# Performance work log

Hardware: AMD Instinct MI355X
Metric: run time of the kernel (lower is better)

Reference implementation:

```python
import jax, jax.numpy as jnp
import numpy as np

B, IN, OUT, NUM_F = 131072, 128, 128, 8


def setup_inputs() -> dict:
    key = jax.random.key(0)
    ks = jax.random.split(key, 6)
    x = jax.random.normal(ks[0], (B, IN), dtype=jnp.float32)
    grid = jnp.arange(NUM_F, dtype=jnp.float32) + 1.0            # nn.Parameter(arange(num_f)+1)
    base_weight = jax.random.normal(ks[1], (OUT, IN), dtype=jnp.float32) * 0.05
    scale_sp = jnp.ones((OUT,), dtype=jnp.float32)
    coef = jax.random.uniform(ks[2], (IN, NUM_F), dtype=jnp.float32)  # torch.rand
    # Conv1d(in=IN*NUM_F, out=OUT*NUM_F, k=1, groups=NUM_F) == per-frequency [OUT, IN] matmul
    fan_in = IN  # per-group in-channels * kernel_size(1)
    bound = 1.0 / np.sqrt(fan_in)
    conv_w = jax.random.uniform(ks[3], (NUM_F, OUT, IN), dtype=jnp.float32,
                                minval=-bound, maxval=bound)
    conv_b = jax.random.uniform(ks[4], (NUM_F, OUT), dtype=jnp.float32,
                                minval=-bound, maxval=bound)
    return {"x": x, "grid": grid, "base_weight": base_weight,
            "scale_sp": scale_sp, "coef": coef, "conv_w": conv_w, "conv_b": conv_b}


def reference(x, grid, base_weight, scale_sp, coef, conv_w, conv_b):
    # base path: SiLU(x) @ W_base^T  -> [B, OUT]
    base_out = jax.nn.silu(x) @ base_weight.T
    # Fourier basis: sin(grid_f * x_i) -> [B, F, I]
    s = jnp.sin(x[:, None, :] * grid[None, :, None])
    # coef [I, F] broadcast-multiplied per (i, f)
    s = s * coef.T[None, :, :]                      # [B, F, I]
    # grouped 1x1 conv == per-frequency matmul, plus per-(f, o) bias
    spline = jnp.einsum('bfi,foi->bfo', s, conv_w) + conv_b[None, :, :]  # [B, F, OUT]
    spline_out = spline.sum(axis=1) * scale_sp      # [B, OUT]
    return base_out + spline_out
```

## Files before the change

kernel.cpp:

```cpp
#include <hip/hip_runtime.h>
#include <stdint.h>

#define NCHUNK 9
#define IN_DIM 128
#define OUT_DIM 128
#define NUM_F 8
#define B_TOTAL 131072

#define WBASE_ELEMS (OUT_DIM * IN_DIM)
#define WSIN_ELEMS (8 * OUT_DIM * IN_DIM)
#define SLICE 16384

typedef _Float16 hf16x8 __attribute__((ext_vector_type(8)));
typedef float floatx16 __attribute__((ext_vector_type(16)));

typedef __attribute__((address_space(1))) const unsigned int gas_u32;
typedef __attribute__((address_space(3))) unsigned int las_u32;

__device__ __forceinline__ unsigned short f2h_rn(float f) {
  _Float16 h = (_Float16)f;
  return __builtin_bit_cast(unsigned short, h);
}

__global__ void skan_prep(const float* __restrict__ base_w,
                          const float* __restrict__ scale_sp,
                          const float* __restrict__ coef,
                          const float* __restrict__ conv_w,
                          const float* __restrict__ conv_b,
                          unsigned short* __restrict__ Wbase,
                          unsigned short* __restrict__ Wsin,
                          float* __restrict__ bias) {
  int b = blockIdx.x;
  int i = threadIdx.x;
  int j = i & 7, q2 = (i >> 3) & 1;
  if (b < NCHUNK * OUT_DIM) {
    int c = b >> 7;
    int o = b & 127;
    if (c == 0) {
      float v = base_w[o * IN_DIM + i];
      Wbase[((i >> 4) * 2 + q2) * 1024 + o * 8 + j] = f2h_rn(v);
    } else {
      int f = c - 1;
      float v = conv_w[(f * OUT_DIM + o) * IN_DIM + i] * coef[i * NUM_F + f] * scale_sp[o];
      Wsin[((i >> 4) * 16 + f * 2 + q2) * 1024 + o * 8 + j] = f2h_rn(v);
    }
  } else {
    float s = 0.f;
#pragma unroll
    for (int f = 0; f < NUM_F; ++f) s += conv_b[f * OUT_DIM + i];
    bias[i] = s * scale_sp[i];
  }
}

__device__ __forceinline__ hf16x8 hpack(const float* v) {
  union { unsigned u[4]; hf16x8 f; } r;
  r.u[0] = __builtin_bit_cast(unsigned, __builtin_amdgcn_cvt_pkrtz(v[0], v[1]));
  r.u[1] = __builtin_bit_cast(unsigned, __builtin_amdgcn_cvt_pkrtz(v[2], v[3]));
  r.u[2] = __builtin_bit_cast(unsigned, __builtin_amdgcn_cvt_pkrtz(v[4], v[5]));
  r.u[3] = __builtin_bit_cast(unsigned, __builtin_amdgcn_cvt_pkrtz(v[6], v[7]));
  return r.f;
}

__device__ __forceinline__ float silu(float v) {
  return v * __builtin_amdgcn_rcpf(1.f + __expf(-v));
}

__global__ __launch_bounds__(256, 3)
void skan_main(const float* __restrict__ x,
               const unsigned short* __restrict__ Wbase,
               const unsigned short* __restrict__ Wsin,
               const float* __restrict__ bias,
               float* __restrict__ out) {
  __shared__ unsigned short sB[SLICE];

  const int tid  = threadIdx.x;
  const int lane = tid & 63;
  const int w    = tid >> 6;
  const int m    = lane & 31;
  const int q2   = lane >> 5;
  const int waveRow = blockIdx.x * 128 + w * 32;

  const int colOff = m * 8;

  floatx16 acc[4];
#pragma unroll
  for (int nt = 0; nt < 4; ++nt)
#pragma unroll
    for (int e = 0; e < 16; ++e) acc[nt][e] = 0.f;

  const float* xr = x + (size_t)(waveRow + m) * IN_DIM;

#pragma unroll 1
  for (int p = 0; p < 8; ++p) {
    {
      const char* src = (const char*)(Wsin + p * SLICE);
      char* dst = (char*)sB;
      int off = tid * 16;
#pragma unroll
      for (int it = 0; it < 8; ++it) {
        __builtin_amdgcn_global_load_lds((gas_u32*)(src + off), (las_u32*)(dst + off),
                                         16, 0, 0);
        off += 4096;
      }
    }

    float xv[8];
    {
      float4 a = *(const float4*)(xr + p * 16 + q2 * 8);
      float4 b = *(const float4*)(xr + p * 16 + q2 * 8 + 4);
      xv[0] = a.x; xv[1] = a.y; xv[2] = a.z; xv[3] = a.w;
      xv[4] = b.x; xv[5] = b.y; xv[6] = b.z; xv[7] = b.w;
    }

    {
      int4 Bb[4];
#pragma unroll
      for (int nt = 0; nt < 4; ++nt)
        Bb[nt] = *(const int4*)(Wbase + (p * 2 + q2) * 1024 + colOff + nt * 256);
      float sv[8];
#pragma unroll
      for (int j = 0; j < 8; ++j) sv[j] = silu(xv[j]);
      hf16x8 a0 = hpack(sv);
#pragma unroll
      for (int nt = 0; nt < 4; ++nt) {
        hf16x8 bf = __builtin_bit_cast(hf16x8, Bb[nt]);
        acc[nt] = __builtin_amdgcn_mfma_f32_32x32x16_f16(a0, bf, acc[nt], 0, 0, 0);
      }
    }

    __syncthreads();

    {
      float sp[8], spp[8], c2[8];
#pragma unroll
      for (int j = 0; j < 8; ++j) {
        float xx = xv[j];
        sp[j]  = __sinf(xx);
        c2[j]  = 2.f * __cosf(xx);
        spp[j] = 0.f;
      }

#pragma unroll
      for (int c = 1; c <= 8; ++c) {
        hf16x8 Bf[4];
        const unsigned short* bp = sB + ((c - 1) * 2 + q2) * 1024 + colOff;
#pragma unroll
        for (int nt = 0; nt < 4; ++nt)
          Bf[nt] = *(const hf16x8*)(bp + nt * 256);

        if (c >= 2) {
#pragma unroll
          for (int j = 0; j < 8; ++j) {
            float t = __builtin_fmaf(c2[j], sp[j], -spp[j]);
            spp[j] = sp[j];
            sp[j] = t;
          }
        }
        hf16x8 a0 = hpack(sp);
#pragma unroll
        for (int nt = 0; nt < 4; ++nt)
          acc[nt] = __builtin_amdgcn_mfma_f32_32x32x16_f16(a0, Bf[nt], acc[nt], 0, 0, 0);
      }
    }

    __syncthreads();
  }

  float* obase = out + (size_t)waveRow * OUT_DIM + m;
#pragma unroll
  for (int nt = 0; nt < 4; ++nt) {
    float bv = bias[nt * 32 + m];
#pragma unroll
    for (int e = 0; e < 16; ++e) {
      int rl = (e & 3) + 8 * (e >> 2) + 4 * q2;
      obase[(size_t)rl * OUT_DIM + nt * 32] = acc[nt][e] + bv;
    }
  }
}

extern "C" void kernel_launch(void* const* d_in, const int* in_sizes, int n_in,
                              void* d_out, int out_size, void* d_ws, size_t ws_size,
                              hipStream_t stream) {
  const float* x      = (const float*)d_in[0];
  const float* base_w = (const float*)d_in[2];
  const float* scale  = (const float*)d_in[3];
  const float* coef   = (const float*)d_in[4];
  const float* conv_w = (const float*)d_in[5];
  const float* conv_b = (const float*)d_in[6];

  unsigned short* Wbase = (unsigned short*)d_ws;
  unsigned short* Wsin  = Wbase + WBASE_ELEMS;
  float* bias = (float*)(Wsin + WSIN_ELEMS);
  float* out  = (float*)d_out;

  skan_prep<<<NCHUNK * OUT_DIM + 1, 128, 0, stream>>>(base_w, scale, coef,
                                                      conv_w, conv_b, Wbase, Wsin, bias);
  skan_main<<<B_TOTAL / 128, 256, 0, stream>>>(x, Wbase, Wsin, bias, out);
}
```

Baseline: 158.9 us.

## Double-buffer sine weight slices in LDS to overlap loads with MFMA

Splits each per-p 32KB sine-weight slice into two 16KB units and stages them into a two-buffer LDS ring. The next unit's global-to-LDS copy is issued while the MFMAs consume the current one, coordinated with explicit vmcnt waits and barriers. s_setprio is raised around the MFMA groups. The aim is to hide weight-load latency that previously stalled each iteration, at the cost of handwritten waitcnt bookkeeping that depends on the exact count of outstanding loads.

```diff
diff --git a/kernel.cpp b/kernel.cpp
--- a/kernel.cpp
+++ b/kernel.cpp
@@ -9,7 +9,7 @@
 
 #define WBASE_ELEMS (OUT_DIM * IN_DIM)
 #define WSIN_ELEMS (8 * OUT_DIM * IN_DIM)
-#define SLICE 16384
+#define UNIT 8192
 
 typedef _Float16 hf16x8 __attribute__((ext_vector_type(8)));
 typedef float floatx16 __attribute__((ext_vector_type(16)));
@@ -71,7 +71,7 @@
                const unsigned short* __restrict__ Wsin,
                const float* __restrict__ bias,
                float* __restrict__ out) {
-  __shared__ unsigned short sB[SLICE];
+  __shared__ unsigned short sB[2][UNIT];
 
   const int tid  = threadIdx.x;
   const int lane = tid & 63;
@@ -90,20 +90,22 @@
 
   const float* xr = x + (size_t)(waveRow + m) * IN_DIM;
 
+  auto stage_unit = [&](int U) {
+    const char* src = (const char*)(Wsin + (size_t)U * UNIT);
+    char* dst = (char*)&sB[U & 1][0];
+    int off = tid * 16;
+#pragma unroll
+    for (int it = 0; it < 4; ++it) {
+      __builtin_amdgcn_global_load_lds((gas_u32*)(src + off), (las_u32*)(dst + off),
+                                       16, 0, 0);
+      off += 4096;
+    }
+  };
+
+  stage_unit(0);
+
 #pragma unroll 1
   for (int p = 0; p < 8; ++p) {
-    {
-      const char* src = (const char*)(Wsin + p * SLICE);
-      char* dst = (char*)sB;
-      int off = tid * 16;
-#pragma unroll
-      for (int it = 0; it < 8; ++it) {
-        __builtin_amdgcn_global_load_lds((gas_u32*)(src + off), (las_u32*)(dst + off),
-                                         16, 0, 0);
-        off += 4096;
-      }
-    }
-
     float xv[8];
     {
       float4 a = *(const float4*)(xr + p * 16 + q2 * 8);
@@ -111,59 +113,89 @@
       xv[0] = a.x; xv[1] = a.y; xv[2] = a.z; xv[3] = a.w;
       xv[4] = b.x; xv[5] = b.y; xv[6] = b.z; xv[7] = b.w;
     }
+    int4 Bb[4];
+#pragma unroll
+    for (int nt = 0; nt < 4; ++nt)
+      Bb[nt] = *(const int4*)(Wbase + (p * 2 + q2) * 1024 + colOff + nt * 256);
+
+    asm volatile("s_waitcnt vmcnt(6)" ::: "memory");
+    __builtin_amdgcn_s_barrier();
+    __builtin_amdgcn_sched_barrier(0);
+    stage_unit(2 * p + 1);
+    __builtin_amdgcn_sched_barrier(0);
 
     {
-      int4 Bb[4];
-#pragma unroll
-      for (int nt = 0; nt < 4; ++nt)
-        Bb[nt] = *(const int4*)(Wbase + (p * 2 + q2) * 1024 + colOff + nt * 256);
       float sv[8];
 #pragma unroll
       for (int j = 0; j < 8; ++j) sv[j] = silu(xv[j]);
       hf16x8 a0 = hpack(sv);
+      __builtin_amdgcn_s_setprio(1);
 #pragma unroll
       for (int nt = 0; nt < 4; ++nt) {
         hf16x8 bf = __builtin_bit_cast(hf16x8, Bb[nt]);
         acc[nt] = __builtin_amdgcn_mfma_f32_32x32x16_f16(a0, bf, acc[nt], 0, 0, 0);
       }
-    }
-
-    __syncthreads();
-
-    {
-      float sp[8], spp[8], c2[8];
+      __builtin_amdgcn_s_setprio(0);
+    }
+
+    float sp[8], spp[8], c2[8];
+#pragma unroll
+    for (int j = 0; j < 8; ++j) {
+      float xx = xv[j];
+      sp[j]  = __sinf(xx);
+      c2[j]  = 2.f * __cosf(xx);
+      spp[j] = 0.f;
+    }
+
+#pragma unroll
+    for (int cc = 0; cc < 4; ++cc) {
+      hf16x8 Bf[4];
+      const unsigned short* bp = &sB[0][(cc * 2 + q2) * 1024 + colOff];
+#pragma unroll
+      for (int nt = 0; nt < 4; ++nt)
+        Bf[nt] = *(const hf16x8*)(bp + nt * 256);
+      if (cc >= 1) {
+#pragma unroll
+        for (int j = 0; j < 8; ++j) {
+          float t = __builtin_fmaf(c2[j], sp[j], -spp[j]);
+          spp[j] = sp[j];
+          sp[j] = t;
+        }
+      }
+      hf16x8 a0 = hpack(sp);
+      __builtin_amdgcn_s_setprio(1);
+#pragma unroll
+      for (int nt = 0; nt < 4; ++nt)
+        acc[nt] = __builtin_amdgcn_mfma_f32_32x32x16_f16(a0, Bf[nt], acc[nt], 0, 0, 0);
+      __builtin_amdgcn_s_setprio(0);
+    }
+
+    asm volatile("s_waitcnt vmcnt(0)" ::: "memory");
+    __builtin_amdgcn_s_barrier();
+    __builtin_amdgcn_sched_barrier(0);
+    if (p < 7) stage_unit(2 * p + 2);
+    __builtin_amdgcn_sched_barrier(0);
+
+#pragma unroll
+    for (int cc = 0; cc < 4; ++cc) {
+      hf16x8 Bf[4];
+      const unsigned short* bp = &sB[1][(cc * 2 + q2) * 1024 + colOff];
+#pragma unroll
+      for (int nt = 0; nt < 4; ++nt)
+        Bf[nt] = *(const hf16x8*)(bp + nt * 256);
 #pragma unroll
       for (int j = 0; j < 8; ++j) {
-        float xx = xv[j];
-        sp[j]  = __sinf(xx);
-        c2[j]  = 2.f * __cosf(xx);
-        spp[j] = 0.f;
+        float t = __builtin_fmaf(c2[j], sp[j], -spp[j]);
+        spp[j] = sp[j];
+        sp[j] = t;
       }
-
-#pragma unroll
-      for (int c = 1; c <= 8; ++c) {
-        hf16x8 Bf[4];
-        const unsigned short* bp = sB + ((c - 1) * 2 + q2) * 1024 + colOff;
-#pragma unroll
-        for (int nt = 0; nt < 4; ++nt)
-          Bf[nt] = *(const hf16x8*)(bp + nt * 256);
-
-        if (c >= 2) {
-#pragma unroll
-          for (int j = 0; j < 8; ++j) {
-            float t = __builtin_fmaf(c2[j], sp[j], -spp[j]);
-            spp[j] = sp[j];
-            sp[j] = t;
-          }
-        }
-        hf16x8 a0 = hpack(sp);
-#pragma unroll
-        for (int nt = 0; nt < 4; ++nt)
-          acc[nt] = __builtin_amdgcn_mfma_f32_32x32x16_f16(a0, Bf[nt], acc[nt], 0, 0, 0);
-      }
-    }
-
-    __syncthreads();
+      hf16x8 a0 = hpack(sp);
+      __builtin_amdgcn_s_setprio(1);
+#pragma unroll
+      for (int nt = 0; nt < 4; ++nt)
+        acc[nt] = __builtin_amdgcn_mfma_f32_32x32x16_f16(a0, Bf[nt], acc[nt], 0, 0, 0);
+      __builtin_amdgcn_s_setprio(0);
+    }
   }
 
   float* obase = out + (size_t)waveRow * OUT_DIM + m;
```

Result: no change. 159.6 us (+0.5%).
